# Kernel tuning notes

Measured on AMD Instinct MI355X. Metric: run time of the kernel, lower is better.

Reference implementation:

```python
import jax, jax.numpy as jnp
import numpy as np

B, T, D, H = 8, 2048, 1024, 1024

def setup_inputs() -> dict:
    key = jax.random.key(0)
    k1, k2, k3, k4 = jax.random.split(key, 4)
    scale = 1.0 / np.sqrt(D)
    return {
        "x": jax.random.normal(k1, (B, T, D), dtype=jnp.float32),
        "Wq": jax.random.normal(k2, (D, H), dtype=jnp.float32) * scale,
        "Wk": jax.random.normal(k3, (D, H), dtype=jnp.float32) * scale,
        "Wv": jax.random.normal(k4, (D, H), dtype=jnp.float32) * scale,
    }

def reference(x, Wq, Wk, Wv):
    # Single-head causal self-attention (dropout in eval mode = identity)
    q = jnp.einsum('btd,dh->bth', x, Wq)
    k = jnp.einsum('btd,dh->bth', x, Wk)
    v = jnp.einsum('btd,dh->bth', x, Wv)
    inv_sqrt_h = 1.0 / jnp.sqrt(jnp.asarray(q.shape[-1], q.dtype))
    scores = jnp.einsum('bqh,bkh->bqk', q, k) * inv_sqrt_h  # [B, T, T]
    Tq = scores.shape[-1]
    causal = jnp.tril(jnp.ones((Tq, Tq), dtype=bool))
    scores = jnp.where(causal, scores, jnp.asarray(-jnp.inf, scores.dtype))
    weights = jax.nn.softmax(scores, axis=-1)
    return jnp.einsum('bqk,bkh->bqh', weights, v)
```

## Files before the change

kernel.cpp:

```cpp
#include <hip/hip_runtime.h>

#define Bn 8
#define Tn 2048
#define Dn 1024
#define Hn 1024
#define Mn (Bn * Tn)

typedef __attribute__((ext_vector_type(8))) short bf16x8;
typedef __attribute__((ext_vector_type(4))) short short4v;
typedef __attribute__((ext_vector_type(4))) float f32x4;

__device__ __forceinline__ unsigned short f2bf(float f) {
  union { float f; unsigned int u; } v; v.f = f;
  unsigned int u = v.u;
  u += 0x7FFFu + ((u >> 16) & 1u);
  return (unsigned short)(u >> 16);
}
__device__ __forceinline__ float bf2f(unsigned short h) {
  union { unsigned int u; float f; } v; v.u = ((unsigned int)h) << 16;
  return v.f;
}

__device__ __forceinline__ void gload_lds16(const unsigned short* g, unsigned short* l) {
  __builtin_amdgcn_global_load_lds((const __attribute__((address_space(1))) void*)g,
                                   (__attribute__((address_space(3))) void*)l, 16, 0, 0);
}

__device__ __forceinline__ void stage128x32(const unsigned short* gbase, size_t row_stride,
                                            unsigned short* lds, int wave, int lane) {
#pragma unroll
  for (int c = 0; c < 2; ++c) {
    const unsigned short* g =
        gbase + (size_t)(wave * 32 + c * 16 + (lane >> 2)) * row_stride + (lane & 3) * 8;
    gload_lds16(g, lds + (wave * 32 + c * 16) * 32);
  }
}

__global__ __launch_bounds__(256) void k_convert(const float* __restrict__ in,
                                                 unsigned short* __restrict__ out, int n4) {
  int idx = blockIdx.x * 256 + threadIdx.x;
  if (idx >= n4) return;
  float4 v = ((const float4*)in)[idx];
  short4v o;
  o.x = (short)f2bf(v.x); o.y = (short)f2bf(v.y);
  o.z = (short)f2bf(v.z); o.w = (short)f2bf(v.w);
  *(short4v*)(out + (size_t)idx * 4) = o;
}

__global__ __launch_bounds__(256) void k_cvt_w_t(const float* __restrict__ W,
                                                 unsigned short* __restrict__ Wt) {
  const int n0 = blockIdx.x * 64, k0 = blockIdx.y * 64;
  __shared__ unsigned short lT[64 * 65];
  const int tid = threadIdx.x;
#pragma unroll
  for (int p = 0; p < 2; ++p) {
    int o = tid + p * 256;
    int r = o >> 3, c = (o & 7) * 8;
    const float* src = W + (size_t)(k0 + r) * Hn + n0 + c;
    float4 v0 = *(const float4*)src;
    float4 v1 = *(const float4*)(src + 4);
    unsigned short* d = &lT[r * 65 + c];
    d[0] = f2bf(v0.x); d[1] = f2bf(v0.y); d[2] = f2bf(v0.z); d[3] = f2bf(v0.w);
    d[4] = f2bf(v1.x); d[5] = f2bf(v1.y); d[6] = f2bf(v1.z); d[7] = f2bf(v1.w);
  }
  __syncthreads();
#pragma unroll
  for (int p = 0; p < 2; ++p) {
    int o = tid + p * 256;
    int r2 = o >> 3, c2 = (o & 7) * 8;
    bf16x8 v;
#pragma unroll
    for (int s = 0; s < 8; ++s) v[s] = (short)lT[(c2 + s) * 65 + r2];
    *(bf16x8*)(Wt + (size_t)(n0 + r2) * Dn + k0 + c2) = v;
  }
}


__global__ __launch_bounds__(256) void gemm_proj(const unsigned short* __restrict__ A,
                                                 const unsigned short* __restrict__ B,
                                                 unsigned short* __restrict__ C, int tr) {
  const int f = blockIdx.x;
  const int c = f & 7;
  const int q = f >> 3;
  const int n0 = (q & 7) * 128;
  const int m0 = ((q >> 3) * 8 + c) * 128;
  __shared__ unsigned short lA[128 * 32];
  __shared__ unsigned short lB[128 * 32];
  const int tid = threadIdx.x;
  const int lane = tid & 63, wave = tid >> 6;
  const int wr = (wave >> 1) * 64, wc = (wave & 1) * 64;
  const int quad = lane >> 4, l16 = lane & 15;

  f32x4 acc[4][4];
#pragma unroll
  for (int i = 0; i < 4; ++i)
#pragma unroll
    for (int j = 0; j < 4; ++j) acc[i][j] = (f32x4){0.f, 0.f, 0.f, 0.f};

  for (int kt = 0; kt < Dn / 32; ++kt) {
    stage128x32(A + (size_t)m0 * Dn + kt * 32, Dn, lA, wave, lane);
    stage128x32(B + (size_t)n0 * Dn + kt * 32, Dn, lB, wave, lane);
    __syncthreads();
    bf16x8 af[4], bfr[4];
#pragma unroll
    for (int i = 0; i < 4; ++i) af[i] = *(const bf16x8*)&lA[(wr + i * 16 + l16) * 32 + quad * 8];
#pragma unroll
    for (int j = 0; j < 4; ++j) bfr[j] = *(const bf16x8*)&lB[(wc + j * 16 + l16) * 32 + quad * 8];
#pragma unroll
    for (int i = 0; i < 4; ++i)
#pragma unroll
      for (int j = 0; j < 4; ++j)
        acc[i][j] = __builtin_amdgcn_mfma_f32_16x16x32_bf16(af[i], bfr[j], acc[i][j], 0, 0, 0);
    __syncthreads();
  }
  if (!tr) {
#pragma unroll
    for (int i = 0; i < 4; ++i)
#pragma unroll
      for (int j = 0; j < 4; ++j)
#pragma unroll
        for (int r = 0; r < 4; ++r) {
          int row = m0 + wr + i * 16 + quad * 4 + r;
          int col = n0 + wc + j * 16 + l16;
          C[(size_t)row * Hn + col] = f2bf(acc[i][j][r]);
        }
  } else {
    const int bb = m0 >> 11;
    const int tb = m0 & 2047;
#pragma unroll
    for (int i = 0; i < 4; ++i)
#pragma unroll
      for (int j = 0; j < 4; ++j) {
        int t0 = tb + wr + i * 16 + quad * 4;
        int h = n0 + wc + j * 16 + l16;
        short4v o;
        o.x = (short)f2bf(acc[i][j][0]);
        o.y = (short)f2bf(acc[i][j][1]);
        o.z = (short)f2bf(acc[i][j][2]);
        o.w = (short)f2bf(acc[i][j][3]);
        *(short4v*)(C + ((size_t)bb * Hn + h) * Tn + t0) = o;
      }
  }
}

__global__ __launch_bounds__(256) void gemm_scores(const unsigned short* __restrict__ Q,
                                                   const unsigned short* __restrict__ K,
                                                   unsigned short* __restrict__ S) {
  const int f = blockIdx.x;
  const int b = f & 7;
  const int q = f >> 3;
  const int rt = 15 - (q & 15);
  const int ct = q >> 4;
  if (ct > rt) return;
  const int j0 = ct * 128, i0 = rt * 128;
  const unsigned short* Qb = Q + (size_t)b * Tn * Hn;
  const unsigned short* Kb = K + (size_t)b * Tn * Hn;
  unsigned short* Sb = S + (size_t)b * Tn * Tn;
  __shared__ unsigned short lA[128 * 32];
  __shared__ unsigned short lB[128 * 32];
  const int tid = threadIdx.x;
  const int lane = tid & 63, wave = tid >> 6;
  const int wr = (wave >> 1) * 64, wc = (wave & 1) * 64;
  const int quad = lane >> 4, l16 = lane & 15;

  f32x4 acc[4][4];
#pragma unroll
  for (int i = 0; i < 4; ++i)
#pragma unroll
    for (int j = 0; j < 4; ++j) acc[i][j] = (f32x4){0.f, 0.f, 0.f, 0.f};

  for (int kt = 0; kt < Hn / 32; ++kt) {
    stage128x32(Qb + (size_t)i0 * Hn + kt * 32, Hn, lA, wave, lane);
    stage128x32(Kb + (size_t)j0 * Hn + kt * 32, Hn, lB, wave, lane);
    __syncthreads();
    bf16x8 af[4], bfr[4];
#pragma unroll
    for (int i = 0; i < 4; ++i) af[i] = *(const bf16x8*)&lA[(wr + i * 16 + l16) * 32 + quad * 8];
#pragma unroll
    for (int j = 0; j < 4; ++j) bfr[j] = *(const bf16x8*)&lB[(wc + j * 16 + l16) * 32 + quad * 8];
#pragma unroll
    for (int i = 0; i < 4; ++i)
#pragma unroll
      for (int j = 0; j < 4; ++j)
        acc[i][j] = __builtin_amdgcn_mfma_f32_16x16x32_bf16(af[i], bfr[j], acc[i][j], 0, 0, 0);
    __syncthreads();
  }
#pragma unroll
  for (int i = 0; i < 4; ++i)
#pragma unroll
    for (int j = 0; j < 4; ++j)
#pragma unroll
      for (int r = 0; r < 4; ++r) {
        int row = i0 + wr + i * 16 + quad * 4 + r;
        int col = j0 + wc + j * 16 + l16;
        float e = (col <= row) ? __expf(acc[i][j][r] * 0.03125f) : 0.f;
        Sb[(size_t)row * Tn + col] = f2bf(e);
      }
}

__global__ __launch_bounds__(256) void k_rowsum(const unsigned short* __restrict__ S,
                                                float* __restrict__ l) {
  const int b = blockIdx.y;
  const int i = blockIdx.x * 4 + (threadIdx.x >> 6);
  const int lane = threadIdx.x & 63;
  const unsigned short* row = S + ((size_t)b * Tn + i) * (size_t)Tn;
  const int npad = ((i >> 7) + 1) << 7;
  float s = 0.f;
  for (int j0 = 0; j0 < npad; j0 += 512) {
    int j = j0 + lane * 8;
    if (j < npad) {
      bf16x8 v = *(const bf16x8*)(row + j);
#pragma unroll
      for (int t = 0; t < 8; ++t) s += bf2f((unsigned short)v[t]);
    }
  }
#pragma unroll
  for (int off = 32; off > 0; off >>= 1) s += __shfl_down(s, off);
  if (lane == 0) l[(size_t)b * Tn + i] = s;
}

__global__ __launch_bounds__(256) void gemm_out(const unsigned short* __restrict__ P,
                                                const unsigned short* __restrict__ Vt,
                                                const float* __restrict__ lbuf,
                                                float* __restrict__ O) {
  const int f = blockIdx.x;
  const int b = f & 7;
  const int q = f >> 3;
  const int n0 = (q & 7) * 128;
  const int rt = 15 - (q >> 3);
  const int i0 = rt * 128;
  const int nkt = rt * 4 + 4;
  const unsigned short* Pb = P + (size_t)b * Tn * Tn;
  const unsigned short* Vb = Vt + (size_t)b * Tn * Hn;
  __shared__ unsigned short lA[128 * 32];
  __shared__ unsigned short lB[128 * 32];
  const int tid = threadIdx.x;
  const int lane = tid & 63, wave = tid >> 6;
  const int wr = (wave >> 1) * 64, wc = (wave & 1) * 64;
  const int quad = lane >> 4, l16 = lane & 15;

  f32x4 acc[4][4];
#pragma unroll
  for (int i = 0; i < 4; ++i)
#pragma unroll
    for (int j = 0; j < 4; ++j) acc[i][j] = (f32x4){0.f, 0.f, 0.f, 0.f};

  for (int kt = 0; kt < nkt; ++kt) {
    stage128x32(Pb + (size_t)i0 * Tn + kt * 32, Tn, lA, wave, lane);
    stage128x32(Vb + (size_t)n0 * Tn + kt * 32, Tn, lB, wave, lane);
    __syncthreads();
    bf16x8 af[4], bfr[4];
#pragma unroll
    for (int i = 0; i < 4; ++i) af[i] = *(const bf16x8*)&lA[(wr + i * 16 + l16) * 32 + quad * 8];
#pragma unroll
    for (int j = 0; j < 4; ++j) bfr[j] = *(const bf16x8*)&lB[(wc + j * 16 + l16) * 32 + quad * 8];
#pragma unroll
    for (int i = 0; i < 4; ++i)
#pragma unroll
      for (int j = 0; j < 4; ++j)
        acc[i][j] = __builtin_amdgcn_mfma_f32_16x16x32_bf16(af[i], bfr[j], acc[i][j], 0, 0, 0);
    __syncthreads();
  }
  float linv[4][4];
#pragma unroll
  for (int i = 0; i < 4; ++i)
#pragma unroll
    for (int r = 0; r < 4; ++r)
      linv[i][r] = 1.f / lbuf[(size_t)b * Tn + (i0 + wr + i * 16 + quad * 4 + r)];
#pragma unroll
  for (int i = 0; i < 4; ++i)
#pragma unroll
    for (int j = 0; j < 4; ++j)
#pragma unroll
      for (int r = 0; r < 4; ++r) {
        int row = i0 + wr + i * 16 + quad * 4 + r;
        int col = n0 + wc + j * 16 + l16;
        O[((size_t)b * Tn + row) * Hn + col] = acc[i][j][r] * linv[i][r];
      }
}

extern "C" void kernel_launch(void* const* d_in, const int* in_sizes, int n_in,
                              void* d_out, int out_size, void* d_ws, size_t ws_size,
                              hipStream_t stream) {
  const float* x  = (const float*)d_in[0];
  const float* Wq = (const float*)d_in[1];
  const float* Wk = (const float*)d_in[2];
  const float* Wv = (const float*)d_in[3];
  float* out = (float*)d_out;

  char* ws = (char*)d_ws;
  const size_t MiB = 1024 * 1024;
  unsigned short* Wtq = (unsigned short*)(ws + 0 * MiB);
  unsigned short* Wtk = (unsigned short*)(ws + 2 * MiB);
  unsigned short* Wtv = (unsigned short*)(ws + 4 * MiB);
  unsigned short* xb  = (unsigned short*)(ws + 6 * MiB);
  unsigned short* Qb  = (unsigned short*)(ws + 38 * MiB);
  unsigned short* Kb  = (unsigned short*)(ws + 70 * MiB);
  unsigned short* Vt  = (unsigned short*)(ws + 102 * MiB);
  unsigned short* S   = (unsigned short*)(ws + 134 * MiB);
  float*          lrow = (float*)(ws + 6 * MiB);

  {
    int n4 = (Mn * Dn) / 4;
    k_convert<<<dim3(n4 / 256), 256, 0, stream>>>(x, xb, n4);
  }
  {
    dim3 g(Hn / 64, Dn / 64);
    k_cvt_w_t<<<g, 256, 0, stream>>>(Wq, Wtq);
    k_cvt_w_t<<<g, 256, 0, stream>>>(Wk, Wtk);
    k_cvt_w_t<<<g, 256, 0, stream>>>(Wv, Wtv);
  }
  {
    gemm_proj<<<dim3(1024), 256, 0, stream>>>(xb, Wtq, Qb, 0);
    gemm_proj<<<dim3(1024), 256, 0, stream>>>(xb, Wtk, Kb, 0);
    gemm_proj<<<dim3(1024), 256, 0, stream>>>(xb, Wtv, Vt, 1);
  }
  {
    gemm_scores<<<dim3(2048), 256, 0, stream>>>(Qb, Kb, S);
  }
  {
    k_rowsum<<<dim3(Tn / 4, Bn), 256, 0, stream>>>(S, lrow);
  }
  {
    gemm_out<<<dim3(1024), 256, 0, stream>>>(S, Vt, lrow, out);
  }
}
```

Before: 403.1 us.

## Fuse QKV projections into one launch and deepen K-tile to 64

The three projection GEMMs become a single 3072-block launch that reads the transposed weights from one contiguous buffer and picks Q, K or transposed V output per block. All GEMM kernels (qkv, scores, output) now stage a 64-wide K slab into two LDS halves per iteration, halving the number of barrier pairs and loop trips. The cost is double the LDS per block, which may reduce occupancy. The combined launch also removes two kernel launches and lets blocks from all three projections share x tiles in cache.

Result: faster. 368.8 us (-8.5%).

```diff
diff --git a/kernel.cpp b/kernel.cpp
--- a/kernel.cpp
+++ b/kernel.cpp
@@ -34,6 +34,13 @@
         gbase + (size_t)(wave * 32 + c * 16 + (lane >> 2)) * row_stride + (lane & 3) * 8;
     gload_lds16(g, lds + (wave * 32 + c * 16) * 32);
   }
+}
+
+__device__ __forceinline__ void stage128x64(const unsigned short* gbase, size_t row_stride,
+                                            unsigned short* lds0, unsigned short* lds1,
+                                            int wave, int lane) {
+  stage128x32(gbase, row_stride, lds0, wave, lane);
+  stage128x32(gbase + 32, row_stride, lds1, wave, lane);
 }
 
 __global__ __launch_bounds__(256) void k_convert(const float* __restrict__ in,
@@ -75,17 +82,21 @@
   }
 }
 
-
-__global__ __launch_bounds__(256) void gemm_proj(const unsigned short* __restrict__ A,
-                                                 const unsigned short* __restrict__ B,
-                                                 unsigned short* __restrict__ C, int tr) {
+__global__ __launch_bounds__(256) void gemm_qkv(const unsigned short* __restrict__ A,
+                                                const unsigned short* __restrict__ Wt3,
+                                                unsigned short* __restrict__ Q,
+                                                unsigned short* __restrict__ Kb,
+                                                unsigned short* __restrict__ Vt) {
   const int f = blockIdx.x;
   const int c = f & 7;
   const int q = f >> 3;
-  const int n0 = (q & 7) * 128;
-  const int m0 = ((q >> 3) * 8 + c) * 128;
-  __shared__ unsigned short lA[128 * 32];
-  __shared__ unsigned short lB[128 * 32];
+  const int nn = q % 24;
+  const int w = nn >> 3;
+  const int n0 = (nn & 7) * 128;
+  const int m0 = ((q / 24) * 8 + c) * 128;
+  const unsigned short* B = Wt3 + (size_t)w * Hn * Dn;
+  __shared__ unsigned short lA[2][128 * 32];
+  __shared__ unsigned short lB[2][128 * 32];
   const int tid = threadIdx.x;
   const int lane = tid & 63, wave = tid >> 6;
   const int wr = (wave >> 1) * 64, wc = (wave & 1) * 64;
@@ -97,23 +108,27 @@
 #pragma unroll
     for (int j = 0; j < 4; ++j) acc[i][j] = (f32x4){0.f, 0.f, 0.f, 0.f};
 
-  for (int kt = 0; kt < Dn / 32; ++kt) {
-    stage128x32(A + (size_t)m0 * Dn + kt * 32, Dn, lA, wave, lane);
-    stage128x32(B + (size_t)n0 * Dn + kt * 32, Dn, lB, wave, lane);
-    __syncthreads();
-    bf16x8 af[4], bfr[4];
-#pragma unroll
-    for (int i = 0; i < 4; ++i) af[i] = *(const bf16x8*)&lA[(wr + i * 16 + l16) * 32 + quad * 8];
-#pragma unroll
-    for (int j = 0; j < 4; ++j) bfr[j] = *(const bf16x8*)&lB[(wc + j * 16 + l16) * 32 + quad * 8];
-#pragma unroll
-    for (int i = 0; i < 4; ++i)
-#pragma unroll
-      for (int j = 0; j < 4; ++j)
-        acc[i][j] = __builtin_amdgcn_mfma_f32_16x16x32_bf16(af[i], bfr[j], acc[i][j], 0, 0, 0);
-    __syncthreads();
-  }
-  if (!tr) {
+  for (int kt = 0; kt < Dn / 64; ++kt) {
+    stage128x64(A + (size_t)m0 * Dn + kt * 64, Dn, lA[0], lA[1], wave, lane);
+    stage128x64(B + (size_t)n0 * Dn + kt * 64, Dn, lB[0], lB[1], wave, lane);
+    __syncthreads();
+#pragma unroll
+    for (int s = 0; s < 2; ++s) {
+      bf16x8 af[4], bfr[4];
+#pragma unroll
+      for (int i = 0; i < 4; ++i) af[i] = *(const bf16x8*)&lA[s][(wr + i * 16 + l16) * 32 + quad * 8];
+#pragma unroll
+      for (int j = 0; j < 4; ++j) bfr[j] = *(const bf16x8*)&lB[s][(wc + j * 16 + l16) * 32 + quad * 8];
+#pragma unroll
+      for (int i = 0; i < 4; ++i)
+#pragma unroll
+        for (int j = 0; j < 4; ++j)
+          acc[i][j] = __builtin_amdgcn_mfma_f32_16x16x32_bf16(af[i], bfr[j], acc[i][j], 0, 0, 0);
+    }
+    __syncthreads();
+  }
+  if (w != 2) {
+    unsigned short* C = (w == 0) ? Q : Kb;
 #pragma unroll
     for (int i = 0; i < 4; ++i)
 #pragma unroll
@@ -138,7 +153,7 @@
         o.y = (short)f2bf(acc[i][j][1]);
         o.z = (short)f2bf(acc[i][j][2]);
         o.w = (short)f2bf(acc[i][j][3]);
-        *(short4v*)(C + ((size_t)bb * Hn + h) * Tn + t0) = o;
+        *(short4v*)(Vt + ((size_t)bb * Hn + h) * Tn + t0) = o;
       }
   }
 }
@@ -156,8 +171,8 @@
   const unsigned short* Qb = Q + (size_t)b * Tn * Hn;
   const unsigned short* Kb = K + (size_t)b * Tn * Hn;
   unsigned short* Sb = S + (size_t)b * Tn * Tn;
-  __shared__ unsigned short lA[128 * 32];
-  __shared__ unsigned short lB[128 * 32];
+  __shared__ unsigned short lA[2][128 * 32];
+  __shared__ unsigned short lB[2][128 * 32];
   const int tid = threadIdx.x;
   const int lane = tid & 63, wave = tid >> 6;
   const int wr = (wave >> 1) * 64, wc = (wave & 1) * 64;
@@ -169,20 +184,23 @@
 #pragma unroll
     for (int j = 0; j < 4; ++j) acc[i][j] = (f32x4){0.f, 0.f, 0.f, 0.f};
 
-  for (int kt = 0; kt < Hn / 32; ++kt) {
-    stage128x32(Qb + (size_t)i0 * Hn + kt * 32, Hn, lA, wave, lane);
-    stage128x32(Kb + (size_t)j0 * Hn + kt * 32, Hn, lB, wave, lane);
-    __syncthreads();
-    bf16x8 af[4], bfr[4];
-#pragma unroll
-    for (int i = 0; i < 4; ++i) af[i] = *(const bf16x8*)&lA[(wr + i * 16 + l16) * 32 + quad * 8];
-#pragma unroll
-    for (int j = 0; j < 4; ++j) bfr[j] = *(const bf16x8*)&lB[(wc + j * 16 + l16) * 32 + quad * 8];
-#pragma unroll
-    for (int i = 0; i < 4; ++i)
-#pragma unroll
-      for (int j = 0; j < 4; ++j)
-        acc[i][j] = __builtin_amdgcn_mfma_f32_16x16x32_bf16(af[i], bfr[j], acc[i][j], 0, 0, 0);
+  for (int kt = 0; kt < Hn / 64; ++kt) {
+    stage128x64(Qb + (size_t)i0 * Hn + kt * 64, Hn, lA[0], lA[1], wave, lane);
+    stage128x64(Kb + (size_t)j0 * Hn + kt * 64, Hn, lB[0], lB[1], wave, lane);
+    __syncthreads();
+#pragma unroll
+    for (int s = 0; s < 2; ++s) {
+      bf16x8 af[4], bfr[4];
+#pragma unroll
+      for (int i = 0; i < 4; ++i) af[i] = *(const bf16x8*)&lA[s][(wr + i * 16 + l16) * 32 + quad * 8];
+#pragma unroll
+      for (int j = 0; j < 4; ++j) bfr[j] = *(const bf16x8*)&lB[s][(wc + j * 16 + l16) * 32 + quad * 8];
+#pragma unroll
+      for (int i = 0; i < 4; ++i)
+#pragma unroll
+        for (int j = 0; j < 4; ++j)
+          acc[i][j] = __builtin_amdgcn_mfma_f32_16x16x32_bf16(af[i], bfr[j], acc[i][j], 0, 0, 0);
+    }
     __syncthreads();
   }
 #pragma unroll
@@ -229,11 +247,11 @@
   const int n0 = (q & 7) * 128;
   const int rt = 15 - (q >> 3);
   const int i0 = rt * 128;
-  const int nkt = rt * 4 + 4;
+  const int nkt = (rt + 1) * 2;
   const unsigned short* Pb = P + (size_t)b * Tn * Tn;
   const unsigned short* Vb = Vt + (size_t)b * Tn * Hn;
-  __shared__ unsigned short lA[128 * 32];
-  __shared__ unsigned short lB[128 * 32];
+  __shared__ unsigned short lA[2][128 * 32];
+  __shared__ unsigned short lB[2][128 * 32];
   const int tid = threadIdx.x;
   const int lane = tid & 63, wave = tid >> 6;
   const int wr = (wave >> 1) * 64, wc = (wave & 1) * 64;
@@ -246,19 +264,22 @@
     for (int j = 0; j < 4; ++j) acc[i][j] = (f32x4){0.f, 0.f, 0.f, 0.f};
 
   for (int kt = 0; kt < nkt; ++kt) {
-    stage128x32(Pb + (size_t)i0 * Tn + kt * 32, Tn, lA, wave, lane);
-    stage128x32(Vb + (size_t)n0 * Tn + kt * 32, Tn, lB, wave, lane);
-    __syncthreads();
-    bf16x8 af[4], bfr[4];
-#pragma unroll
-    for (int i = 0; i < 4; ++i) af[i] = *(const bf16x8*)&lA[(wr + i * 16 + l16) * 32 + quad * 8];
-#pragma unroll
-    for (int j = 0; j < 4; ++j) bfr[j] = *(const bf16x8*)&lB[(wc + j * 16 + l16) * 32 + quad * 8];
-#pragma unroll
-    for (int i = 0; i < 4; ++i)
-#pragma unroll
-      for (int j = 0; j < 4; ++j)
-        acc[i][j] = __builtin_amdgcn_mfma_f32_16x16x32_bf16(af[i], bfr[j], acc[i][j], 0, 0, 0);
+    stage128x64(Pb + (size_t)i0 * Tn + kt * 64, Tn, lA[0], lA[1], wave, lane);
+    stage128x64(Vb + (size_t)n0 * Tn + kt * 64, Tn, lB[0], lB[1], wave, lane);
+    __syncthreads();
+#pragma unroll
+    for (int s = 0; s < 2; ++s) {
+      bf16x8 af[4], bfr[4];
+#pragma unroll
+      for (int i = 0; i < 4; ++i) af[i] = *(const bf16x8*)&lA[s][(wr + i * 16 + l16) * 32 + quad * 8];
+#pragma unroll
+      for (int j = 0; j < 4; ++j) bfr[j] = *(const bf16x8*)&lB[s][(wc + j * 16 + l16) * 32 + quad * 8];
+#pragma unroll
+      for (int i = 0; i < 4; ++i)
+#pragma unroll
+        for (int j = 0; j < 4; ++j)
+          acc[i][j] = __builtin_amdgcn_mfma_f32_16x16x32_bf16(af[i], bfr[j], acc[i][j], 0, 0, 0);
+    }
     __syncthreads();
   }
   float linv[4][4];
@@ -290,9 +311,7 @@
 
   char* ws = (char*)d_ws;
   const size_t MiB = 1024 * 1024;
-  unsigned short* Wtq = (unsigned short*)(ws + 0 * MiB);
-  unsigned short* Wtk = (unsigned short*)(ws + 2 * MiB);
-  unsigned short* Wtv = (unsigned short*)(ws + 4 * MiB);
+  unsigned short* Wt3 = (unsigned short*)(ws + 0 * MiB);
   unsigned short* xb  = (unsigned short*)(ws + 6 * MiB);
   unsigned short* Qb  = (unsigned short*)(ws + 38 * MiB);
   unsigned short* Kb  = (unsigned short*)(ws + 70 * MiB);
@@ -306,14 +325,12 @@
   }
   {
     dim3 g(Hn / 64, Dn / 64);
-    k_cvt_w_t<<<g, 256, 0, stream>>>(Wq, Wtq);
-    k_cvt_w_t<<<g, 256, 0, stream>>>(Wk, Wtk);
-    k_cvt_w_t<<<g, 256, 0, stream>>>(Wv, Wtv);
-  }
-  {
-    gemm_proj<<<dim3(1024), 256, 0, stream>>>(xb, Wtq, Qb, 0);
-    gemm_proj<<<dim3(1024), 256, 0, stream>>>(xb, Wtk, Kb, 0);
-    gemm_proj<<<dim3(1024), 256, 0, stream>>>(xb, Wtv, Vt, 1);
+    k_cvt_w_t<<<g, 256, 0, stream>>>(Wq, Wt3);
+    k_cvt_w_t<<<g, 256, 0, stream>>>(Wk, Wt3 + (size_t)Hn * Dn);
+    k_cvt_w_t<<<g, 256, 0, stream>>>(Wv, Wt3 + (size_t)2 * Hn * Dn);
+  }
+  {
+    gemm_qkv<<<dim3(3072), 256, 0, stream>>>(xb, Wt3, Qb, Kb, Vt);
   }
   {
     gemm_scores<<<dim3(2048), 256, 0, stream>>>(Qb, Kb, S);
```
